# Kernel tuning notes

Measured on AMD Instinct MI355X. Metric: run time of the kernel, lower is better.

## Reference

```python
import jax, jax.numpy as jnp
import numpy as np

B, S, IN = 4096, 2048, 8
H, LIN, A = 8, 4, 4

def _lstm_cell(x, h, c, Wih, Whh, bih, bhh):
    # torch gate order: i, f, g, o ; gates: [B, 4H]
    gates = x @ Wih.T + h @ Whh.T + bih + bhh
    i, f, g, o = jnp.split(gates, 4, axis=-1)
    i = jax.nn.sigmoid(i); f = jax.nn.sigmoid(f)
    g = jnp.tanh(g);       o = jax.nn.sigmoid(o)
    c = f * c + i * g
    h = o * jnp.tanh(c)
    return h, c

def setup_inputs() -> dict:
    key = jax.random.key(0)
    ks = jax.random.split(key, 20)
    seq = jax.random.normal(ks[0], (B, S, IN), dtype=jnp.float32)
    lengths = jax.random.randint(ks[1], (B,), 1, S + 1, dtype=jnp.int32)
    def w(k, shape, scale=0.1):
        return (jax.random.normal(k, shape, dtype=jnp.float32) * scale)
    return {
        "seq": seq, "lengths": lengths,
        # LSTM layer 0 (input 8 -> hidden 8)
        "Wih0": w(ks[2], (4 * H, IN)), "Whh0": w(ks[3], (4 * H, H)),
        "bih0": w(ks[4], (4 * H,)),   "bhh0": w(ks[5], (4 * H,)),
        # LSTM layer 1 (hidden 8 -> hidden 8)
        "Wih1": w(ks[6], (4 * H, H)), "Whh1": w(ks[7], (4 * H, H)),
        "bih1": w(ks[8], (4 * H,)),  "bhh1": w(ks[9], (4 * H,)),
        # heads
        "Wl": w(ks[10], (LIN, H)),  "bl": w(ks[11], (LIN,)),
        "Wv": w(ks[12], (1, LIN)),  "bv": jnp.zeros((1,), jnp.float32),
        "Wa": w(ks[13], (A, LIN)),  "ba": jnp.zeros((A,), jnp.float32),
        "log_std": jnp.zeros((1, A), jnp.float32),
    }

def reference(seq, lengths, Wih0, Whh0, bih0, bhh0, Wih1, Whh1, bih1, bhh1,
              Wl, bl, Wv, bv, Wa, ba, log_std):
    b = seq.shape[0]
    xs = jnp.transpose(seq, (1, 0, 2))  # [S, B, IN] time-major for scan
    z = jnp.zeros((b, H), seq.dtype)

    def step(carry, x_t):
        h0, c0, h1, c1 = carry
        h0, c0 = _lstm_cell(x_t, h0, c0, Wih0, Whh0, bih0, bhh0)
        h1, c1 = _lstm_cell(h0, h1, c1, Wih1, Whh1, bih1, bhh1)
        return (h0, c0, h1, c1), h1

    _, outs = jax.lax.scan(step, (z, z, z, z), xs)  # outs: [S, B, H]
    # packed-sequence semantics: take the last VALID output per sequence
    y = outs[lengths - 1, jnp.arange(b)]            # [B, H]
    feat = jnp.tanh(y @ Wl.T + bl)                  # [B, LIN]
    value = feat @ Wv.T + bv                        # [B, 1]
    action_mean = feat @ Wa.T + ba                  # [B, A]
    action_log_std = jnp.broadcast_to(log_std, action_mean.shape)
    action_std = jnp.exp(action_log_std)
    return value, action_mean, action_log_std, action_std
```

## Files before the change

kernel.cpp:

```cpp
#include <hip/hip_runtime.h>

#define B_ 4096
#define S_ 2048
#define CH 8

typedef float v2f __attribute__((ext_vector_type(2)));

__device__ __forceinline__ float rcp_(float x)  { return __builtin_amdgcn_rcpf(x); }
__device__ __forceinline__ float exp2_(float x) { return __builtin_amdgcn_exp2f(x); }
__device__ __forceinline__ float tanh_(float x) {
    return fmaf(-2.0f, rcp_(1.0f + exp2_(2.88539008f * x)), 1.0f);
}
template<int CTRL>
__device__ __forceinline__ float dppf(float x) {
    int v = __builtin_bit_cast(int, x);
    return __builtin_bit_cast(float,
        __builtin_amdgcn_update_dpp(v, v, CTRL, 0xF, 0xF, false));
}
#define ROR2f dppf<0x122>
__device__ __forceinline__ int dppi_ror2(int x) {
    return __builtin_amdgcn_update_dpp(x, x, 0x122, 0xF, 0xF, false);
}

#define L2E 1.44269504f

__global__ __launch_bounds__(384) void lstm_main(
    const float* __restrict__ seq, const int* __restrict__ lengths,
    const float* __restrict__ Wih0, const float* __restrict__ Whh0,
    const float* __restrict__ bih0, const float* __restrict__ bhh0,
    const float* __restrict__ Wih1, const float* __restrict__ Whh1,
    const float* __restrict__ bih1, const float* __restrict__ bhh1,
    const float* __restrict__ Wl, const float* __restrict__ bl,
    const float* __restrict__ Wv, const float* __restrict__ bv,
    const float* __restrict__ Wa, const float* __restrict__ ba,
    const float* __restrict__ lstd, float* __restrict__ out)
{
    __shared__ float  ring0[2][CH][64];
    __shared__ float4 ringX[2][CH][8][8];
    __shared__ float4 ringY[2][CH][8][8];

    const int tid = threadIdx.x;
    const int wv  = tid >> 6;
    const int l   = tid & 63;
    const int p   = l & 1;
    const int j   = (l >> 1) & 7;
    const int sq  = (l >> 4) * 2 + p;
    const int b   = blockIdx.x * 8 + sq;

    const int probe = dppi_ror2(j);
    const int delta = (j - probe) & 7;

    v2f wA[8], wB[8];
    v2f biasA = (v2f){0.0f, 0.0f}, biasB = (v2f){0.0f, 0.0f};
    if (wv < 2) {
        const float* Whh = (wv == 0) ? Whh0 : Whh1;
        int idx = j;
        #pragma unroll
        for (int k = 0; k < 8; ++k) {
            wA[k] = (v2f){ Whh[(j)      * 8 + idx] * -L2E,
                           Whh[(8 + j)  * 8 + idx] * -L2E };
            wB[k] = (v2f){ Whh[(16 + j) * 8 + idx] * (2.0f * L2E),
                           Whh[(24 + j) * 8 + idx] * -L2E };
            idx = (idx - delta) & 7;
        }
    } else {
        const bool l0 = (wv <= 3);
        const float* Wih = l0 ? Wih0 : Wih1;
        const float* bi  = l0 ? bih0 : bih1;
        const float* bh  = l0 ? bhh0 : bhh1;
        #pragma unroll
        for (int k = 0; k < 8; ++k) {
            wA[k] = (v2f){ Wih[(j)      * 8 + k] * -L2E,
                           Wih[(8 + j)  * 8 + k] * -L2E };
            wB[k] = (v2f){ Wih[(16 + j) * 8 + k] * (2.0f * L2E),
                           Wih[(24 + j) * 8 + k] * -L2E };
        }
        biasA = (v2f){ (bi[j]      + bh[j])      * -L2E,
                       (bi[8 + j]  + bh[8 + j])  * -L2E };
        biasB = (v2f){ (bi[16 + j] + bh[16 + j]) * (2.0f * L2E),
                       (bi[24 + j] + bh[24 + j]) * -L2E };
    }

    const int len   = lengths[b];
    const int lenm1 = len - 1;
    int maxlen = len;
    maxlen = max(maxlen, __shfl_xor(maxlen, 1));
    maxlen = max(maxlen, __shfl_xor(maxlen, 16));
    maxlen = max(maxlen, __shfl_xor(maxlen, 32));
    const int nch = (maxlen + CH - 1) / CH;

    float hq = 0.0f, cq = 0.0f, ysave = 0.0f;
    const float* xbase = seq + (size_t)b * S_ * 8;
    const int s0 = (wv == 2 || wv == 4) ? 0 : 4;

    for (int k = 0; k <= nch + 2; ++k) {
        if (wv >= 2) {
            if (wv <= 3) {
                if (k < nch) {
                    const int t0 = k * CH;
                    #pragma unroll
                    for (int s = s0; s < s0 + 4; ++s) {
                        const float* xp = xbase + (size_t)(t0 + s) * 8;
                        const float4 xa = *(const float4*)xp;
                        const float4 xb = *(const float4*)(xp + 4);
                        float xv[8] = {xa.x, xa.y, xa.z, xa.w, xb.x, xb.y, xb.z, xb.w};
                        v2f aA = biasA, aB = biasB;
                        #pragma unroll
                        for (int q = 0; q < 8; ++q) {
                            aA += wA[q] * (v2f){xv[q], xv[q]};
                            aB += wB[q] * (v2f){xv[q], xv[q]};
                        }
                        ringX[k & 1][s][sq][j] = make_float4(aA.x, aA.y, aB.x, aB.y);
                    }
                }
            } else {
                const int c = k - 2;
                if (c >= 0 && c < nch) {
                    #pragma unroll
                    for (int s = s0; s < s0 + 4; ++s) {
                        const float4 ha = *(const float4*)&ring0[c & 1][s][sq * 8];
                        const float4 hb = *(const float4*)&ring0[c & 1][s][sq * 8 + 4];
                        float hv[8] = {ha.x, ha.y, ha.z, ha.w, hb.x, hb.y, hb.z, hb.w};
                        v2f aA = biasA, aB = biasB;
                        #pragma unroll
                        for (int q = 0; q < 8; ++q) {
                            aA += wA[q] * (v2f){hv[q], hv[q]};
                            aB += wB[q] * (v2f){hv[q], hv[q]};
                        }
                        ringY[c & 1][s][sq][j] = make_float4(aA.x, aA.y, aB.x, aB.y);
                    }
                }
            }
        } else if (wv == 0) {
            const int c = k - 1;
            if (c >= 0 && c < nch) {
                float4 xg[CH];
                #pragma unroll
                for (int s = 0; s < CH; ++s) xg[s] = ringX[c & 1][s][sq][j];
                #pragma unroll
                for (int s = 0; s < CH; ++s) {
                    v2f aA = (v2f){xg[s].x, xg[s].y};
                    v2f aB = (v2f){xg[s].z, xg[s].w};
                    float rr = hq;
                    #pragma unroll
                    for (int q = 0; q < 8; ++q) {
                        aA += wA[q] * (v2f){rr, rr};
                        aB += wB[q] * (v2f){rr, rr};
                        if (q < 7) rr = ROR2f(rr);
                    }
                    float si = rcp_(1.0f + exp2_(aA.x));
                    float sf = rcp_(1.0f + exp2_(aA.y));
                    float tg = fmaf(-2.0f, rcp_(1.0f + exp2_(aB.x)), 1.0f);
                    float so = rcp_(1.0f + exp2_(aB.y));
                    cq = fmaf(sf, cq, si * tg);
                    hq = so * tanh_(cq);
                    ring0[c & 1][s][sq * 8 + j] = hq;
                }
            }
        } else {
            const int c = k - 3;
            if (c >= 0 && c < nch) {
                float4 yg[CH];
                #pragma unroll
                for (int s = 0; s < CH; ++s) yg[s] = ringY[c & 1][s][sq][j];
                const int u0 = c * CH;
                #pragma unroll
                for (int s = 0; s < CH; ++s) {
                    v2f aA = (v2f){yg[s].x, yg[s].y};
                    v2f aB = (v2f){yg[s].z, yg[s].w};
                    float rr = hq;
                    #pragma unroll
                    for (int q = 0; q < 8; ++q) {
                        aA += wA[q] * (v2f){rr, rr};
                        aB += wB[q] * (v2f){rr, rr};
                        if (q < 7) rr = ROR2f(rr);
                    }
                    float si = rcp_(1.0f + exp2_(aA.x));
                    float sf = rcp_(1.0f + exp2_(aA.y));
                    float tg = fmaf(-2.0f, rcp_(1.0f + exp2_(aB.x)), 1.0f);
                    float so = rcp_(1.0f + exp2_(aB.y));
                    cq = fmaf(sf, cq, si * tg);
                    hq = so * tanh_(cq);
                    ysave = (u0 + s == lenm1) ? hq : ysave;
                }
            }
        }
        __syncthreads();
    }

    if (wv == 1) {
        const int lbase = (l & 48) | p;
        float yv[8];
        #pragma unroll
        for (int k = 0; k < 8; ++k) yv[k] = __shfl(ysave, lbase + 2 * k);
        if (j == 0) {
            float feat[4];
            #pragma unroll
            for (int q = 0; q < 4; ++q) {
                float acc = bl[q];
                #pragma unroll
                for (int k = 0; k < 8; ++k) acc = fmaf(Wl[q * 8 + k], yv[k], acc);
                feat[q] = tanh_(acc);
            }
            float val = bv[0];
            #pragma unroll
            for (int q = 0; q < 4; ++q) val = fmaf(Wv[q], feat[q], val);
            out[b] = val;
            #pragma unroll
            for (int a = 0; a < 4; ++a) {
                float am = ba[a];
                #pragma unroll
                for (int q = 0; q < 4; ++q) am = fmaf(Wa[a * 4 + q], feat[q], am);
                out[4096  + b * 4 + a] = am;
                float ls = lstd[a];
                out[20480 + b * 4 + a] = ls;
                out[36864 + b * 4 + a] = exp2_(L2E * ls);
            }
        }
    }
}

extern "C" void kernel_launch(void* const* d_in, const int* in_sizes, int n_in,
                              void* d_out, int out_size, void* d_ws, size_t ws_size,
                              hipStream_t stream)
{
    const float* seq   = (const float*)d_in[0];
    const int* lengths = (const int*)d_in[1];
    const float* Wih0  = (const float*)d_in[2];
    const float* Whh0  = (const float*)d_in[3];
    const float* bih0  = (const float*)d_in[4];
    const float* bhh0  = (const float*)d_in[5];
    const float* Wih1  = (const float*)d_in[6];
    const float* Whh1  = (const float*)d_in[7];
    const float* bih1  = (const float*)d_in[8];
    const float* bhh1  = (const float*)d_in[9];
    const float* Wl    = (const float*)d_in[10];
    const float* bl    = (const float*)d_in[11];
    const float* Wv    = (const float*)d_in[12];
    const float* bv    = (const float*)d_in[13];
    const float* Wa    = (const float*)d_in[14];
    const float* ba    = (const float*)d_in[15];
    const float* lstd  = (const float*)d_in[16];

    lstm_main<<<B_ / 8, 384, 0, stream>>>(seq, lengths, Wih0, Whh0, bih0, bhh0,
                                          Wih1, Whh1, bih1, bhh1,
                                          Wl, bl, Wv, bv, Wa, ba, lstd,
                                          (float*)d_out);
}
```

Measured before the change: 799.2 us.

## Double block to 16 sequences, prefetch inputs, prioritize recurrent waves, merge gate reciprocals

Each block now covers 16 sequences with 12 waves: four heavy recurrent waves (two per layer) and eight projection waves. The projection waves feeding layer 0 prefetch the next chunk's inputs into registers so the global loads overlap the barrier wait. The recurrent waves get a raised scheduling priority, and the gate math folds the input-gate and tanh reciprocals into one rcp to shorten the serial chain. In exchange, maxlen is now taken over 16 sequences, which can add padded steps, and register pressure and occupancy change under the 768-thread launch bound.

```diff
diff --git a/kernel.cpp b/kernel.cpp
--- a/kernel.cpp
+++ b/kernel.cpp
@@ -21,10 +21,16 @@
 __device__ __forceinline__ int dppi_ror2(int x) {
     return __builtin_amdgcn_update_dpp(x, x, 0x122, 0xF, 0xF, false);
 }
+__device__ __forceinline__ void ld8(const float* p, float* o) {
+    float4 a = *(const float4*)p;
+    float4 b = *(const float4*)(p + 4);
+    o[0] = a.x; o[1] = a.y; o[2] = a.z; o[3] = a.w;
+    o[4] = b.x; o[5] = b.y; o[6] = b.z; o[7] = b.w;
+}
 
 #define L2E 1.44269504f
 
-__global__ __launch_bounds__(384) void lstm_main(
+__global__ __launch_bounds__(768) void lstm_main(
     const float* __restrict__ seq, const int* __restrict__ lengths,
     const float* __restrict__ Wih0, const float* __restrict__ Whh0,
     const float* __restrict__ bih0, const float* __restrict__ bhh0,
@@ -35,25 +41,40 @@
     const float* __restrict__ Wa, const float* __restrict__ ba,
     const float* __restrict__ lstd, float* __restrict__ out)
 {
-    __shared__ float  ring0[2][CH][64];
-    __shared__ float4 ringX[2][CH][8][8];
-    __shared__ float4 ringY[2][CH][8][8];
+    __shared__ float  ring0[2][CH][128];
+    __shared__ float4 ringX[2][CH][16][8];
+    __shared__ float4 ringY[2][CH][16][8];
 
     const int tid = threadIdx.x;
     const int wv  = tid >> 6;
     const int l   = tid & 63;
     const int p   = l & 1;
     const int j   = (l >> 1) & 7;
-    const int sq  = (l >> 4) * 2 + p;
-    const int b   = blockIdx.x * 8 + sq;
+    const int s8  = (l >> 4) * 2 + p;
+
+    const bool heavy = (wv % 3) == 0;
+    int layer, sbase, s0 = 0;
+    if (heavy) {
+        const int hid = wv / 3;
+        layer = hid >> 1;
+        sbase = (hid & 1) * 8;
+    } else {
+        layer = (wv >= 7) ? 1 : 0;
+        const int idx = (layer == 0) ? ((wv >= 4) ? (wv - 2) : (wv - 1))
+                                     : ((wv >= 10) ? (wv - 8) : (wv - 7));
+        sbase = (idx >> 1) * 8;
+        s0    = (idx & 1) * 4;
+    }
+    const int sq = sbase + s8;
+    const int b  = blockIdx.x * 16 + sq;
 
     const int probe = dppi_ror2(j);
     const int delta = (j - probe) & 7;
 
     v2f wA[8], wB[8];
     v2f biasA = (v2f){0.0f, 0.0f}, biasB = (v2f){0.0f, 0.0f};
-    if (wv < 2) {
-        const float* Whh = (wv == 0) ? Whh0 : Whh1;
+    if (heavy) {
+        const float* Whh = layer ? Whh1 : Whh0;
         int idx = j;
         #pragma unroll
         for (int k = 0; k < 8; ++k) {
@@ -64,10 +85,9 @@
             idx = (idx - delta) & 7;
         }
     } else {
-        const bool l0 = (wv <= 3);
-        const float* Wih = l0 ? Wih0 : Wih1;
-        const float* bi  = l0 ? bih0 : bih1;
-        const float* bh  = l0 ? bhh0 : bhh1;
+        const float* Wih = layer ? Wih1 : Wih0;
+        const float* bi  = layer ? bih1 : bih0;
+        const float* bh  = layer ? bhh1 : bhh0;
         #pragma unroll
         for (int k = 0; k < 8; ++k) {
             wA[k] = (v2f){ Wih[(j)      * 8 + k] * -L2E,
@@ -81,45 +101,71 @@
                        (bi[24 + j] + bh[24 + j]) * -L2E };
     }
 
-    const int len   = lengths[b];
-    const int lenm1 = len - 1;
-    int maxlen = len;
-    maxlen = max(maxlen, __shfl_xor(maxlen, 1));
-    maxlen = max(maxlen, __shfl_xor(maxlen, 16));
-    maxlen = max(maxlen, __shfl_xor(maxlen, 32));
-    const int nch = (maxlen + CH - 1) / CH;
+    int m = lengths[blockIdx.x * 16 + (l & 15)];
+    m = max(m, __shfl_xor(m, 1));
+    m = max(m, __shfl_xor(m, 2));
+    m = max(m, __shfl_xor(m, 4));
+    m = max(m, __shfl_xor(m, 8));
+    const int nch   = (m + CH - 1) / CH;
+    const int lenm1 = lengths[b] - 1;
 
     float hq = 0.0f, cq = 0.0f, ysave = 0.0f;
     const float* xbase = seq + (size_t)b * S_ * 8;
-    const int s0 = (wv == 2 || wv == 4) ? 0 : 4;
+
+    float xq[4][8];
+    if (!heavy && layer == 0) {
+        #pragma unroll
+        for (int s = 0; s < 4; ++s) ld8(xbase + (size_t)(s0 + s) * 8, xq[s]);
+    }
+    if (heavy) __builtin_amdgcn_s_setprio(1);
+
+    auto rstep = [&](v2f aA, v2f aB) {
+        float rr = hq;
+        #pragma unroll
+        for (int q = 0; q < 8; ++q) {
+            aA += wA[q] * (v2f){rr, rr};
+            aB += wB[q] * (v2f){rr, rr};
+            if (q < 7) rr = ROR2f(rr);
+        }
+        float Ei = exp2_(aA.x);
+        float Ef = exp2_(aA.y);
+        float Eg = exp2_(aB.x);
+        float Eo = exp2_(aB.y);
+        float sf  = rcp_(1.0f + Ef);
+        float itg = (Eg - 1.0f) * rcp_((1.0f + Ei) * (1.0f + Eg));
+        cq = fmaf(sf, cq, itg);
+        float so = rcp_(1.0f + Eo);
+        hq = so * tanh_(cq);
+    };
 
     for (int k = 0; k <= nch + 2; ++k) {
-        if (wv >= 2) {
-            if (wv <= 3) {
+        if (!heavy) {
+            if (layer == 0) {
                 if (k < nch) {
-                    const int t0 = k * CH;
                     #pragma unroll
-                    for (int s = s0; s < s0 + 4; ++s) {
-                        const float* xp = xbase + (size_t)(t0 + s) * 8;
-                        const float4 xa = *(const float4*)xp;
-                        const float4 xb = *(const float4*)(xp + 4);
-                        float xv[8] = {xa.x, xa.y, xa.z, xa.w, xb.x, xb.y, xb.z, xb.w};
+                    for (int s = 0; s < 4; ++s) {
                         v2f aA = biasA, aB = biasB;
                         #pragma unroll
                         for (int q = 0; q < 8; ++q) {
-                            aA += wA[q] * (v2f){xv[q], xv[q]};
-                            aB += wB[q] * (v2f){xv[q], xv[q]};
+                            aA += wA[q] * (v2f){xq[s][q], xq[s][q]};
+                            aB += wB[q] * (v2f){xq[s][q], xq[s][q]};
                         }
-                        ringX[k & 1][s][sq][j] = make_float4(aA.x, aA.y, aB.x, aB.y);
+                        ringX[k & 1][s0 + s][sq][j] = make_float4(aA.x, aA.y, aB.x, aB.y);
+                    }
+                    if (k + 1 < nch) {
+                        const int t0 = (k + 1) * CH + s0;
+                        #pragma unroll
+                        for (int s = 0; s < 4; ++s)
+                            ld8(xbase + (size_t)(t0 + s) * 8, xq[s]);
                     }
                 }
             } else {
                 const int c = k - 2;
                 if (c >= 0 && c < nch) {
                     #pragma unroll
-                    for (int s = s0; s < s0 + 4; ++s) {
-                        const float4 ha = *(const float4*)&ring0[c & 1][s][sq * 8];
-                        const float4 hb = *(const float4*)&ring0[c & 1][s][sq * 8 + 4];
+                    for (int s = 0; s < 4; ++s) {
+                        const float4 ha = *(const float4*)&ring0[c & 1][s0 + s][sq * 8];
+                        const float4 hb = *(const float4*)&ring0[c & 1][s0 + s][sq * 8 + 4];
                         float hv[8] = {ha.x, ha.y, ha.z, ha.w, hb.x, hb.y, hb.z, hb.w};
                         v2f aA = biasA, aB = biasB;
                         #pragma unroll
@@ -127,11 +173,11 @@
                             aA += wA[q] * (v2f){hv[q], hv[q]};
                             aB += wB[q] * (v2f){hv[q], hv[q]};
                         }
-                        ringY[c & 1][s][sq][j] = make_float4(aA.x, aA.y, aB.x, aB.y);
+                        ringY[c & 1][s0 + s][sq][j] = make_float4(aA.x, aA.y, aB.x, aB.y);
                     }
                 }
             }
-        } else if (wv == 0) {
+        } else if (layer == 0) {
             const int c = k - 1;
             if (c >= 0 && c < nch) {
                 float4 xg[CH];
@@ -139,21 +185,7 @@
                 for (int s = 0; s < CH; ++s) xg[s] = ringX[c & 1][s][sq][j];
                 #pragma unroll
                 for (int s = 0; s < CH; ++s) {
-                    v2f aA = (v2f){xg[s].x, xg[s].y};
-                    v2f aB = (v2f){xg[s].z, xg[s].w};
-                    float rr = hq;
-                    #pragma unroll
-                    for (int q = 0; q < 8; ++q) {
-                        aA += wA[q] * (v2f){rr, rr};
-                        aB += wB[q] * (v2f){rr, rr};
-                        if (q < 7) rr = ROR2f(rr);
-                    }
-                    float si = rcp_(1.0f + exp2_(aA.x));
-                    float sf = rcp_(1.0f + exp2_(aA.y));
-                    float tg = fmaf(-2.0f, rcp_(1.0f + exp2_(aB.x)), 1.0f);
-                    float so = rcp_(1.0f + exp2_(aB.y));
-                    cq = fmaf(sf, cq, si * tg);
-                    hq = so * tanh_(cq);
+                    rstep((v2f){xg[s].x, xg[s].y}, (v2f){xg[s].z, xg[s].w});
                     ring0[c & 1][s][sq * 8 + j] = hq;
                 }
             }
@@ -166,21 +198,7 @@
                 const int u0 = c * CH;
                 #pragma unroll
                 for (int s = 0; s < CH; ++s) {
-                    v2f aA = (v2f){yg[s].x, yg[s].y};
-                    v2f aB = (v2f){yg[s].z, yg[s].w};
-                    float rr = hq;
-                    #pragma unroll
-                    for (int q = 0; q < 8; ++q) {
-                        aA += wA[q] * (v2f){rr, rr};
-                        aB += wB[q] * (v2f){rr, rr};
-                        if (q < 7) rr = ROR2f(rr);
-                    }
-                    float si = rcp_(1.0f + exp2_(aA.x));
-                    float sf = rcp_(1.0f + exp2_(aA.y));
-                    float tg = fmaf(-2.0f, rcp_(1.0f + exp2_(aB.x)), 1.0f);
-                    float so = rcp_(1.0f + exp2_(aB.y));
-                    cq = fmaf(sf, cq, si * tg);
-                    hq = so * tanh_(cq);
+                    rstep((v2f){yg[s].x, yg[s].y}, (v2f){yg[s].z, yg[s].w});
                     ysave = (u0 + s == lenm1) ? hq : ysave;
                 }
             }
@@ -188,7 +206,7 @@
         __syncthreads();
     }
 
-    if (wv == 1) {
+    if (heavy && layer == 1) {
         const int lbase = (l & 48) | p;
         float yv[8];
         #pragma unroll
@@ -242,8 +260,8 @@
     const float* ba    = (const float*)d_in[15];
     const float* lstd  = (const float*)d_in[16];
 
-    lstm_main<<<B_ / 8, 384, 0, stream>>>(seq, lengths, Wih0, Whh0, bih0, bhh0,
-                                          Wih1, Whh1, bih1, bhh1,
-                                          Wl, bl, Wv, bv, Wa, ba, lstd,
-                                          (float*)d_out);
-}
+    lstm_main<<<B_ / 16, 768, 0, stream>>>(seq, lengths, Wih0, Whh0, bih0, bhh0,
+                                           Wih1, Whh1, bih1, bhh1,
+                                           Wl, bl, Wv, bv, Wa, ba, lstd,
+                                           (float*)d_out);
+}
```

Result: faster. 647.8 us (-18.9%).
